# Performance work log

Hardware: AMD Instinct MI355X
Metric: run time of the kernel (lower is better)

Reference implementation:

```python
import jax, jax.numpy as jnp
import numpy as np

B, H, T1, T2, DK, DV = 4, 16, 1024, 1024, 64, 64


def setup_inputs() -> dict:
    key = jax.random.key(0)
    k1, k2, k3 = jax.random.split(key, 3)
    return {
        "query": jax.random.normal(k1, (B, H, T1, DK), dtype=jnp.float32),
        "key": jax.random.normal(k2, (B, T2, DK), dtype=jnp.float32),
        "value": jax.random.normal(k3, (B, T2, DV), dtype=jnp.float32),
        "mask": jnp.zeros((T1, T2), dtype=jnp.float32),
    }


def reference(query, key, value, mask):
    # logits = tanh(Q K^T): [B,H,T1,T2]; key broadcast over heads
    logits = jnp.tanh(jnp.einsum("bhqd,bkd->bhqk", query, key))
    logits = logits + mask  # additive positional mask [T1,T2]
    weights = jax.nn.softmax(logits, axis=-1)
    out = jnp.einsum("bhqk,bkv->bhqv", weights, value)
    return out, weights
```

## Files before the change

kernel.cpp:

```cpp
#include <hip/hip_runtime.h>


typedef _Float16 f16;
typedef __attribute__((ext_vector_type(2))) _Float16 f16x2;
typedef __attribute__((ext_vector_type(4))) _Float16 f16x4;
typedef __attribute__((ext_vector_type(8))) _Float16 f16x8;
typedef __attribute__((ext_vector_type(2))) __fp16  fp16x2;
typedef __attribute__((ext_vector_type(4))) float f32x4;

#define LOG2E 1.44269504088896340736f

union U8 { f16x8 v; f16x2 h[4]; };
union U4 { f16x4 v; f16x2 h[2]; };

static __device__ __forceinline__ f16x2 pk(float a, float b) {
  union { fp16x2 src; f16x2 dst; } u;
  u.src = __builtin_amdgcn_cvt_pkrtz(a, b);
  return u.dst;
}

static __device__ __forceinline__ void tanh_exp4(const f32x4& acc, const f32x4& m4,
                                                 float p[4]) {
  #pragma unroll
  for (int i = 0; i < 4; ++i) {
    float x = acc[i];
    float t = __builtin_amdgcn_exp2f(x * (2.0f * LOG2E));
    float r = __builtin_amdgcn_rcpf(t + 1.0f);
    p[i] = __builtin_amdgcn_exp2f(
               fmaf(m4[i], LOG2E, fmaf(r, -2.0f * LOG2E, LOG2E)));
  }
}

__global__ __launch_bounds__(256) void prep(
    const float* __restrict__ K, const float* __restrict__ V,
    const float* __restrict__ M,
    f16* __restrict__ Kp, f16* __restrict__ Vp, float* __restrict__ Mp)
{
  int idx = blockIdx.x * 256 + threadIdx.x;
  if (idx < 32768) {
    int l = idx & 63, ks = (idx >> 6) & 1, fc = (idx >> 7) & 63, b = idx >> 13;
    const float* s = K + ((size_t)b * 1024 + fc * 16 + (l & 15)) * 64
                       + (l >> 4) * 8 + ks * 32;
    f32x4 x = *(const f32x4*)s;
    f32x4 y = *(const f32x4*)(s + 4);
    U8 u;
    u.h[0] = pk(x[0], x[1]); u.h[1] = pk(x[2], x[3]);
    u.h[2] = pk(y[0], y[1]); u.h[3] = pk(y[2], y[3]);
    *(f16x8*)(Kp + (size_t)idx * 8) = u.v;
  } else if (idx < 98304) {
    int t = idx - 32768;
    int l = t & 63, nb = (t >> 6) & 3, fc = (t >> 8) & 63, b = t >> 14;
    const float* s = V + ((size_t)b * 1024 + fc * 16 + (l >> 4) * 4) * 64
                       + nb * 16 + (l & 15);
    U4 u;
    u.h[0] = pk(s[0],   s[64]);
    u.h[1] = pk(s[128], s[192]);
    *(f16x4*)(Vp + (size_t)t * 4) = u.v;
  } else if (idx < 360448) {
    int t = idx - 98304;
    int l = t & 63, fc = (t >> 6) & 63, q16 = t >> 12;
    const float* s = M + ((size_t)q16 * 16 + (l & 15)) * 1024
                       + fc * 16 + (l >> 4) * 4;
    *(f32x4*)(Mp + (size_t)t * 4) = *(const f32x4*)s;
  }
}

__global__ __launch_bounds__(256, 4) void attn_main(
    const float* __restrict__ Q, const f16* __restrict__ Kp,
    const f16* __restrict__ Vp, const float* __restrict__ Mp,
    float* __restrict__ Out, float* __restrict__ W)
{
  const int bh   = blockIdx.x >> 4;
  const int qt   = blockIdx.x & 15;
  const int b    = bh >> 4;
  const int lane = threadIdx.x & 63;
  const int wv   = threadIdx.x >> 6;
  const int qv   = lane & 15;
  const int g    = lane >> 4;
  const int qbase = qt * 64 + wv * 16;

  const float* qp = Q + ((size_t)(bh * 1024 + qbase + qv)) * 64 + g * 8;
  f16x8 bq[2];
  #pragma unroll
  for (int ks = 0; ks < 2; ++ks) {
    f32x4 a = *(const f32x4*)(qp + ks * 32);
    f32x4 c = *(const f32x4*)(qp + ks * 32 + 4);
    U8 u;
    u.h[0] = pk(a[0], a[1]); u.h[1] = pk(a[2], a[3]);
    u.h[2] = pk(c[0], c[1]); u.h[3] = pk(c[2], c[3]);
    bq[ks] = u.v;
  }

  const f16*   kpB = Kp + (size_t)b * 65536 + lane * 8;
  const f16*   vpB = Vp + (size_t)b * 65536 + lane * 4;
  const float* mpB = Mp + (size_t)(qt * 4 + wv) * 16384 + lane * 4;

  float rsum = 0.0f;
  f32x4 oacc[4];
  #pragma unroll
  for (int nb = 0; nb < 4; ++nb) oacc[nb] = f32x4{0.f, 0.f, 0.f, 0.f};

  #pragma unroll 2
  for (int fc = 0; fc < 64; ++fc) {
    f16x8 a0 = *(const f16x8*)(kpB + fc * 1024);
    f16x8 a1 = *(const f16x8*)(kpB + fc * 1024 + 512);
    f32x4 acc = {0.f, 0.f, 0.f, 0.f};
    acc = __builtin_amdgcn_mfma_f32_16x16x32_f16(a0, bq[0], acc, 0, 0, 0);
    acc = __builtin_amdgcn_mfma_f32_16x16x32_f16(a1, bq[1], acc, 0, 0, 0);

    f32x4 m4 = *(const f32x4*)(mpB + fc * 256);
    float p[4];
    tanh_exp4(acc, m4, p);
    rsum += (p[0] + p[1]) + (p[2] + p[3]);

    U4 pu;
    pu.h[0] = pk(p[0], p[1]);
    pu.h[1] = pk(p[2], p[3]);

    #pragma unroll
    for (int nb = 0; nb < 4; ++nb) {
      f16x4 bv = *(const f16x4*)(vpB + fc * 1024 + nb * 256);
      oacc[nb] = __builtin_amdgcn_mfma_f32_16x16x16f16(pu.v, bv, oacc[nb], 0, 0, 0);
    }
  }

  rsum += __shfl_xor(rsum, 16);
  rsum += __shfl_xor(rsum, 32);
  const float rz = 1.0f / rsum;
  float rzq[4];
  #pragma unroll
  for (int i = 0; i < 4; ++i) rzq[i] = __shfl(rz, g * 4 + i);

  float* ol = Out + ((size_t)(bh * 1024 + qbase)) * 64 + qv;
  #pragma unroll
  for (int nb = 0; nb < 4; ++nb) {
    #pragma unroll
    for (int i = 0; i < 4; ++i) {
      ol[(size_t)(g * 4 + i) * 64 + nb * 16] = oacc[nb][i] * rzq[i];
    }
  }

  float* wl = W + ((size_t)(bh * 1024 + qbase + qv)) * 1024 + g * 4;
  #pragma unroll 4
  for (int fc = 0; fc < 64; ++fc) {
    f16x8 a0 = *(const f16x8*)(kpB + fc * 1024);
    f16x8 a1 = *(const f16x8*)(kpB + fc * 1024 + 512);
    f32x4 acc = {0.f, 0.f, 0.f, 0.f};
    acc = __builtin_amdgcn_mfma_f32_16x16x32_f16(a0, bq[0], acc, 0, 0, 0);
    acc = __builtin_amdgcn_mfma_f32_16x16x32_f16(a1, bq[1], acc, 0, 0, 0);

    f32x4 m4 = *(const f32x4*)(mpB + fc * 256);
    float p[4];
    tanh_exp4(acc, m4, p);

    f32x4 w4;
    w4[0] = p[0] * rz; w4[1] = p[1] * rz;
    w4[2] = p[2] * rz; w4[3] = p[3] * rz;
    *(f32x4*)(wl + fc * 16) = w4;
  }
}

__global__ __launch_bounds__(256, 4) void attn_fused(
    const float* __restrict__ Q, const float* __restrict__ K,
    const float* __restrict__ V, const float* __restrict__ M,
    float* __restrict__ Out, float* __restrict__ W)
{
  const int bh   = blockIdx.x >> 4;
  const int qt   = blockIdx.x & 15;
  const int b    = bh >> 4;
  const int lane = threadIdx.x & 63;
  const int wv   = threadIdx.x >> 6;
  const int qv   = lane & 15;
  const int g    = lane >> 4;
  const int qbase = qt * 64 + wv * 16;

  const float* qp = Q + ((size_t)(bh * 1024 + qbase + qv)) * 64 + g * 8;
  f16x8 bq[2];
  #pragma unroll
  for (int ks = 0; ks < 2; ++ks) {
    f32x4 a = *(const f32x4*)(qp + ks * 32);
    f32x4 c = *(const f32x4*)(qp + ks * 32 + 4);
    U8 u;
    u.h[0] = pk(a[0], a[1]); u.h[1] = pk(a[2], a[3]);
    u.h[2] = pk(c[0], c[1]); u.h[3] = pk(c[2], c[3]);
    bq[ks] = u.v;
  }
  const float* kp = K + ((size_t)(b * 1024 + qv)) * 64 + g * 8;
  const float* mp = M + (size_t)(qbase + qv) * 1024 + g * 4;
  const float* vp = V + (size_t)b * 65536 + g * 256 + qv;

  float rsum = 0.0f;
  f32x4 oacc[4];
  #pragma unroll
  for (int nb = 0; nb < 4; ++nb) oacc[nb] = f32x4{0.f, 0.f, 0.f, 0.f};

  #pragma unroll 2
  for (int fc = 0; fc < 64; ++fc) {
    const float* kf = kp + fc * 1024;
    f16x8 ak[2];
    #pragma unroll
    for (int ks = 0; ks < 2; ++ks) {
      f32x4 a = *(const f32x4*)(kf + ks * 32);
      f32x4 c = *(const f32x4*)(kf + ks * 32 + 4);
      U8 u;
      u.h[0] = pk(a[0], a[1]); u.h[1] = pk(a[2], a[3]);
      u.h[2] = pk(c[0], c[1]); u.h[3] = pk(c[2], c[3]);
      ak[ks] = u.v;
    }
    f32x4 acc = {0.f, 0.f, 0.f, 0.f};
    acc = __builtin_amdgcn_mfma_f32_16x16x32_f16(ak[0], bq[0], acc, 0, 0, 0);
    acc = __builtin_amdgcn_mfma_f32_16x16x32_f16(ak[1], bq[1], acc, 0, 0, 0);
    f32x4 m4 = *(const f32x4*)(mp + fc * 16);
    float p[4];
    tanh_exp4(acc, m4, p);
    rsum += (p[0] + p[1]) + (p[2] + p[3]);
    U4 pu;
    pu.h[0] = pk(p[0], p[1]);
    pu.h[1] = pk(p[2], p[3]);
    const float* vf = vp + fc * 1024;
    #pragma unroll
    for (int nb = 0; nb < 4; ++nb) {
      U4 bu;
      bu.h[0] = pk(vf[nb * 16],       vf[nb * 16 + 64]);
      bu.h[1] = pk(vf[nb * 16 + 128], vf[nb * 16 + 192]);
      oacc[nb] = __builtin_amdgcn_mfma_f32_16x16x16f16(pu.v, bu.v, oacc[nb], 0, 0, 0);
    }
  }
  rsum += __shfl_xor(rsum, 16);
  rsum += __shfl_xor(rsum, 32);
  const float rz = 1.0f / rsum;
  float rzq[4];
  #pragma unroll
  for (int i = 0; i < 4; ++i) rzq[i] = __shfl(rz, g * 4 + i);
  float* ol = Out + ((size_t)(bh * 1024 + qbase)) * 64 + qv;
  #pragma unroll
  for (int nb = 0; nb < 4; ++nb)
    #pragma unroll
    for (int i = 0; i < 4; ++i)
      ol[(size_t)(g * 4 + i) * 64 + nb * 16] = oacc[nb][i] * rzq[i];

  float* wl = W + ((size_t)(bh * 1024 + qbase + qv)) * 1024 + g * 4;
  #pragma unroll 2
  for (int fc = 0; fc < 64; ++fc) {
    const float* kf = kp + fc * 1024;
    f16x8 ak[2];
    #pragma unroll
    for (int ks = 0; ks < 2; ++ks) {
      f32x4 a = *(const f32x4*)(kf + ks * 32);
      f32x4 c = *(const f32x4*)(kf + ks * 32 + 4);
      U8 u;
      u.h[0] = pk(a[0], a[1]); u.h[1] = pk(a[2], a[3]);
      u.h[2] = pk(c[0], c[1]); u.h[3] = pk(c[2], c[3]);
      ak[ks] = u.v;
    }
    f32x4 acc = {0.f, 0.f, 0.f, 0.f};
    acc = __builtin_amdgcn_mfma_f32_16x16x32_f16(ak[0], bq[0], acc, 0, 0, 0);
    acc = __builtin_amdgcn_mfma_f32_16x16x32_f16(ak[1], bq[1], acc, 0, 0, 0);
    f32x4 m4 = *(const f32x4*)(mp + fc * 16);
    float p[4];
    tanh_exp4(acc, m4, p);
    f32x4 w4;
    w4[0] = p[0] * rz; w4[1] = p[1] * rz;
    w4[2] = p[2] * rz; w4[3] = p[3] * rz;
    *(f32x4*)(wl + fc * 16) = w4;
  }
}

extern "C" void kernel_launch(void* const* d_in, const int* in_sizes, int n_in,
                              void* d_out, int out_size, void* d_ws, size_t ws_size,
                              hipStream_t stream) {
  const float* Q = (const float*)d_in[0];
  const float* K = (const float*)d_in[1];
  const float* V = (const float*)d_in[2];
  const float* M = (const float*)d_in[3];
  float* Out = (float*)d_out;
  float* W   = Out + (size_t)4 * 16 * 1024 * 64;

  const size_t KP_BYTES = 524288, VP_BYTES = 524288, MP_BYTES = 4194304;
  if (ws_size >= KP_BYTES + VP_BYTES + MP_BYTES) {
    f16*   Kp = (f16*)d_ws;
    f16*   Vp = (f16*)((char*)d_ws + KP_BYTES);
    float* Mp = (float*)((char*)d_ws + KP_BYTES + VP_BYTES);
    hipLaunchKernelGGL(prep, dim3(1408), dim3(256), 0, stream, K, V, M, Kp, Vp, Mp);
    hipLaunchKernelGGL(attn_main, dim3(1024), dim3(256), 0, stream,
                       Q, Kp, Vp, Mp, Out, W);
  } else {
    hipLaunchKernelGGL(attn_fused, dim3(1024), dim3(256), 0, stream,
                       Q, K, V, M, Out, W);
  }
}
```

Before: 374.7 us.

## Split attention into row-sum kernel and fused weights-plus-PV pass

Moves the softmax denominator computation into its own kernel that writes per-row reciprocal sums to workspace. The second kernel then computes logits once, writing normalized weights and accumulating the PV product in the same loop, instead of accumulating PV in one loop and recomputing logits for the weights in another. The QK/tanh/exp work per element is unchanged (still done twice overall), but the weight stores now interleave with the MFMA PV work, and the cost is an extra kernel launch plus a small workspace buffer and an extra Q load. The fast path now needs slightly more workspace, so the fallback may trigger if the workspace is too small.

```diff
diff --git a/kernel.cpp b/kernel.cpp
--- a/kernel.cpp
+++ b/kernel.cpp
@@ -28,6 +28,18 @@
     float r = __builtin_amdgcn_rcpf(t + 1.0f);
     p[i] = __builtin_amdgcn_exp2f(
                fmaf(m4[i], LOG2E, fmaf(r, -2.0f * LOG2E, LOG2E)));
+  }
+}
+
+static __device__ __forceinline__ void load_bq(const float* qp, f16x8 bq[2]) {
+  #pragma unroll
+  for (int ks = 0; ks < 2; ++ks) {
+    f32x4 a = *(const f32x4*)(qp + ks * 32);
+    f32x4 c = *(const f32x4*)(qp + ks * 32 + 4);
+    U8 u;
+    u.h[0] = pk(a[0], a[1]); u.h[1] = pk(a[2], a[3]);
+    u.h[2] = pk(c[0], c[1]); u.h[3] = pk(c[2], c[3]);
+    bq[ks] = u.v;
   }
 }
 
@@ -65,9 +77,47 @@
   }
 }
 
-__global__ __launch_bounds__(256, 4) void attn_main(
+__global__ __launch_bounds__(256, 4) void attn_rsum(
+    const float* __restrict__ Q, const f16* __restrict__ Kp,
+    const float* __restrict__ Mp, float* __restrict__ Rz)
+{
+  const int bh   = blockIdx.x >> 4;
+  const int qt   = blockIdx.x & 15;
+  const int b    = bh >> 4;
+  const int lane = threadIdx.x & 63;
+  const int wv   = threadIdx.x >> 6;
+  const int qv   = lane & 15;
+  const int qbase = qt * 64 + wv * 16;
+
+  const float* qp = Q + ((size_t)(bh * 1024 + qbase + qv)) * 64 + (lane >> 4) * 8;
+  f16x8 bq[2];
+  load_bq(qp, bq);
+
+  const f16*   kpB = Kp + (size_t)b * 65536 + lane * 8;
+  const float* mpB = Mp + (size_t)(qt * 4 + wv) * 16384 + lane * 4;
+
+  float rsum = 0.0f;
+  #pragma unroll 4
+  for (int fc = 0; fc < 64; ++fc) {
+    f16x8 a0 = *(const f16x8*)(kpB + fc * 1024);
+    f16x8 a1 = *(const f16x8*)(kpB + fc * 1024 + 512);
+    f32x4 acc = {0.f, 0.f, 0.f, 0.f};
+    acc = __builtin_amdgcn_mfma_f32_16x16x32_f16(a0, bq[0], acc, 0, 0, 0);
+    acc = __builtin_amdgcn_mfma_f32_16x16x32_f16(a1, bq[1], acc, 0, 0, 0);
+    f32x4 m4 = *(const f32x4*)(mpB + fc * 256);
+    float p[4];
+    tanh_exp4(acc, m4, p);
+    rsum += (p[0] + p[1]) + (p[2] + p[3]);
+  }
+  rsum += __shfl_xor(rsum, 16);
+  rsum += __shfl_xor(rsum, 32);
+  if (lane < 16) Rz[bh * 1024 + qbase + lane] = 1.0f / rsum;
+}
+
+__global__ __launch_bounds__(256, 4) void attn_pass2(
     const float* __restrict__ Q, const f16* __restrict__ Kp,
     const f16* __restrict__ Vp, const float* __restrict__ Mp,
+    const float* __restrict__ Rz,
     float* __restrict__ Out, float* __restrict__ W)
 {
   const int bh   = blockIdx.x >> 4;
@@ -81,21 +131,18 @@
 
   const float* qp = Q + ((size_t)(bh * 1024 + qbase + qv)) * 64 + g * 8;
   f16x8 bq[2];
-  #pragma unroll
-  for (int ks = 0; ks < 2; ++ks) {
-    f32x4 a = *(const f32x4*)(qp + ks * 32);
-    f32x4 c = *(const f32x4*)(qp + ks * 32 + 4);
-    U8 u;
-    u.h[0] = pk(a[0], a[1]); u.h[1] = pk(a[2], a[3]);
-    u.h[2] = pk(c[0], c[1]); u.h[3] = pk(c[2], c[3]);
-    bq[ks] = u.v;
-  }
+  load_bq(qp, bq);
 
   const f16*   kpB = Kp + (size_t)b * 65536 + lane * 8;
   const f16*   vpB = Vp + (size_t)b * 65536 + lane * 4;
   const float* mpB = Mp + (size_t)(qt * 4 + wv) * 16384 + lane * 4;
 
-  float rsum = 0.0f;
+  const float rz = Rz[bh * 1024 + qbase + qv];
+  float rzq[4];
+  #pragma unroll
+  for (int i = 0; i < 4; ++i) rzq[i] = __shfl(rz, g * 4 + i);
+
+  float* wl = W + ((size_t)(bh * 1024 + qbase + qv)) * 1024 + g * 4;
   f32x4 oacc[4];
   #pragma unroll
   for (int nb = 0; nb < 4; ++nb) oacc[nb] = f32x4{0.f, 0.f, 0.f, 0.f};
@@ -111,52 +158,29 @@
     f32x4 m4 = *(const f32x4*)(mpB + fc * 256);
     float p[4];
     tanh_exp4(acc, m4, p);
-    rsum += (p[0] + p[1]) + (p[2] + p[3]);
-
-    U4 pu;
-    pu.h[0] = pk(p[0], p[1]);
-    pu.h[1] = pk(p[2], p[3]);
-
-    #pragma unroll
-    for (int nb = 0; nb < 4; ++nb) {
-      f16x4 bv = *(const f16x4*)(vpB + fc * 1024 + nb * 256);
-      oacc[nb] = __builtin_amdgcn_mfma_f32_16x16x16f16(pu.v, bv, oacc[nb], 0, 0, 0);
-    }
-  }
-
-  rsum += __shfl_xor(rsum, 16);
-  rsum += __shfl_xor(rsum, 32);
-  const float rz = 1.0f / rsum;
-  float rzq[4];
-  #pragma unroll
-  for (int i = 0; i < 4; ++i) rzq[i] = __shfl(rz, g * 4 + i);
-
-  float* ol = Out + ((size_t)(bh * 1024 + qbase)) * 64 + qv;
-  #pragma unroll
-  for (int nb = 0; nb < 4; ++nb) {
-    #pragma unroll
-    for (int i = 0; i < 4; ++i) {
-      ol[(size_t)(g * 4 + i) * 64 + nb * 16] = oacc[nb][i] * rzq[i];
-    }
-  }
-
-  float* wl = W + ((size_t)(bh * 1024 + qbase + qv)) * 1024 + g * 4;
-  #pragma unroll 4
-  for (int fc = 0; fc < 64; ++fc) {
-    f16x8 a0 = *(const f16x8*)(kpB + fc * 1024);
-    f16x8 a1 = *(const f16x8*)(kpB + fc * 1024 + 512);
-    f32x4 acc = {0.f, 0.f, 0.f, 0.f};
-    acc = __builtin_amdgcn_mfma_f32_16x16x32_f16(a0, bq[0], acc, 0, 0, 0);
-    acc = __builtin_amdgcn_mfma_f32_16x16x32_f16(a1, bq[1], acc, 0, 0, 0);
-
-    f32x4 m4 = *(const f32x4*)(mpB + fc * 256);
-    float p[4];
-    tanh_exp4(acc, m4, p);
 
     f32x4 w4;
     w4[0] = p[0] * rz; w4[1] = p[1] * rz;
     w4[2] = p[2] * rz; w4[3] = p[3] * rz;
     *(f32x4*)(wl + fc * 16) = w4;
+
+    U4 pu;
+    pu.h[0] = pk(p[0], p[1]);
+    pu.h[1] = pk(p[2], p[3]);
+    #pragma unroll
+    for (int nb = 0; nb < 4; ++nb) {
+      f16x4 bv = *(const f16x4*)(vpB + fc * 1024 + nb * 256);
+      oacc[nb] = __builtin_amdgcn_mfma_f32_16x16x16f16(pu.v, bv, oacc[nb], 0, 0, 0);
+    }
+  }
+
+  float* ol = Out + ((size_t)(bh * 1024 + qbase)) * 64 + qv;
+  #pragma unroll
+  for (int nb = 0; nb < 4; ++nb) {
+    #pragma unroll
+    for (int i = 0; i < 4; ++i) {
+      ol[(size_t)(g * 4 + i) * 64 + nb * 16] = oacc[nb][i] * rzq[i];
+    }
   }
 }
 
@@ -176,15 +200,7 @@
 
   const float* qp = Q + ((size_t)(bh * 1024 + qbase + qv)) * 64 + g * 8;
   f16x8 bq[2];
-  #pragma unroll
-  for (int ks = 0; ks < 2; ++ks) {
-    f32x4 a = *(const f32x4*)(qp + ks * 32);
-    f32x4 c = *(const f32x4*)(qp + ks * 32 + 4);
-    U8 u;
-    u.h[0] = pk(a[0], a[1]); u.h[1] = pk(a[2], a[3]);
-    u.h[2] = pk(c[0], c[1]); u.h[3] = pk(c[2], c[3]);
-    bq[ks] = u.v;
-  }
+  load_bq(qp, bq);
   const float* kp = K + ((size_t)(b * 1024 + qv)) * 64 + g * 8;
   const float* mp = M + (size_t)(qbase + qv) * 1024 + g * 4;
   const float* vp = V + (size_t)b * 65536 + g * 256 + qv;
@@ -276,14 +292,17 @@
   float* Out = (float*)d_out;
   float* W   = Out + (size_t)4 * 16 * 1024 * 64;
 
-  const size_t KP_BYTES = 524288, VP_BYTES = 524288, MP_BYTES = 4194304;
-  if (ws_size >= KP_BYTES + VP_BYTES + MP_BYTES) {
+  const size_t KP_BYTES = 524288, VP_BYTES = 524288, MP_BYTES = 4194304,
+               RZ_BYTES = 262144;
+  if (ws_size >= KP_BYTES + VP_BYTES + MP_BYTES + RZ_BYTES) {
     f16*   Kp = (f16*)d_ws;
     f16*   Vp = (f16*)((char*)d_ws + KP_BYTES);
     float* Mp = (float*)((char*)d_ws + KP_BYTES + VP_BYTES);
+    float* Rz = (float*)((char*)d_ws + KP_BYTES + VP_BYTES + MP_BYTES);
     hipLaunchKernelGGL(prep, dim3(1408), dim3(256), 0, stream, K, V, M, Kp, Vp, Mp);
-    hipLaunchKernelGGL(attn_main, dim3(1024), dim3(256), 0, stream,
-                       Q, Kp, Vp, Mp, Out, W);
+    hipLaunchKernelGGL(attn_rsum, dim3(1024), dim3(256), 0, stream, Q, Kp, Mp, Rz);
+    hipLaunchKernelGGL(attn_pass2, dim3(1024), dim3(256), 0, stream,
+                       Q, Kp, Vp, Mp, Rz, Out, W);
   } else {
     hipLaunchKernelGGL(attn_fused, dim3(1024), dim3(256), 0, stream,
                        Q, K, V, M, Out, W);
```

New measurement: 384.2 us. +2.5%, slower.

## Split key range across two wave groups per block with LDS reduction

Applied to the files above, without the earlier changes.

Doubles the block to 512 threads so each 16-query subtile is handled by two waves, each covering half of the key chunks. Partial row sums and output accumulators are combined through shared memory after a barrier, and each half then writes its own part of the weights. The goal is more waves in flight and a shorter serial loop per wave. The cost is extra LDS traffic, a block-wide synchronization, and K/V fragments being loaded by more waves.

```diff
diff --git a/kernel.cpp b/kernel.cpp
--- a/kernel.cpp
+++ b/kernel.cpp
@@ -28,6 +28,18 @@
     float r = __builtin_amdgcn_rcpf(t + 1.0f);
     p[i] = __builtin_amdgcn_exp2f(
                fmaf(m4[i], LOG2E, fmaf(r, -2.0f * LOG2E, LOG2E)));
+  }
+}
+
+static __device__ __forceinline__ void load_bq(const float* qp, f16x8 bq[2]) {
+  #pragma unroll
+  for (int ks = 0; ks < 2; ++ks) {
+    f32x4 a = *(const f32x4*)(qp + ks * 32);
+    f32x4 c = *(const f32x4*)(qp + ks * 32 + 4);
+    U8 u;
+    u.h[0] = pk(a[0], a[1]); u.h[1] = pk(a[2], a[3]);
+    u.h[2] = pk(c[0], c[1]); u.h[3] = pk(c[2], c[3]);
+    bq[ks] = u.v;
   }
 }
 
@@ -65,35 +77,33 @@
   }
 }
 
-__global__ __launch_bounds__(256, 4) void attn_main(
+__global__ __launch_bounds__(512, 6) void attn_main2(
     const float* __restrict__ Q, const f16* __restrict__ Kp,
     const f16* __restrict__ Vp, const float* __restrict__ Mp,
     float* __restrict__ Out, float* __restrict__ W)
 {
+  __shared__ float redO[8][16][64];
+  __shared__ float redS[8][16];
+
   const int bh   = blockIdx.x >> 4;
   const int qt   = blockIdx.x & 15;
   const int b    = bh >> 4;
   const int lane = threadIdx.x & 63;
-  const int wv   = threadIdx.x >> 6;
+  const int ww   = threadIdx.x >> 6;
+  const int sub  = ww & 3;
+  const int kh   = ww >> 2;
   const int qv   = lane & 15;
   const int g    = lane >> 4;
-  const int qbase = qt * 64 + wv * 16;
+  const int qbase = qt * 64 + sub * 16;
+  const int fc0 = kh * 32, fc1 = fc0 + 32;
 
   const float* qp = Q + ((size_t)(bh * 1024 + qbase + qv)) * 64 + g * 8;
   f16x8 bq[2];
-  #pragma unroll
-  for (int ks = 0; ks < 2; ++ks) {
-    f32x4 a = *(const f32x4*)(qp + ks * 32);
-    f32x4 c = *(const f32x4*)(qp + ks * 32 + 4);
-    U8 u;
-    u.h[0] = pk(a[0], a[1]); u.h[1] = pk(a[2], a[3]);
-    u.h[2] = pk(c[0], c[1]); u.h[3] = pk(c[2], c[3]);
-    bq[ks] = u.v;
-  }
+  load_bq(qp, bq);
 
   const f16*   kpB = Kp + (size_t)b * 65536 + lane * 8;
   const f16*   vpB = Vp + (size_t)b * 65536 + lane * 4;
-  const float* mpB = Mp + (size_t)(qt * 4 + wv) * 16384 + lane * 4;
+  const float* mpB = Mp + (size_t)(qt * 4 + sub) * 16384 + lane * 4;
 
   float rsum = 0.0f;
   f32x4 oacc[4];
@@ -101,7 +111,7 @@
   for (int nb = 0; nb < 4; ++nb) oacc[nb] = f32x4{0.f, 0.f, 0.f, 0.f};
 
   #pragma unroll 2
-  for (int fc = 0; fc < 64; ++fc) {
+  for (int fc = fc0; fc < fc1; ++fc) {
     f16x8 a0 = *(const f16x8*)(kpB + fc * 1024);
     f16x8 a1 = *(const f16x8*)(kpB + fc * 1024 + 512);
     f32x4 acc = {0.f, 0.f, 0.f, 0.f};
@@ -116,7 +126,6 @@
     U4 pu;
     pu.h[0] = pk(p[0], p[1]);
     pu.h[1] = pk(p[2], p[3]);
-
     #pragma unroll
     for (int nb = 0; nb < 4; ++nb) {
       f16x4 bv = *(const f16x4*)(vpB + fc * 1024 + nb * 256);
@@ -126,23 +135,35 @@
 
   rsum += __shfl_xor(rsum, 16);
   rsum += __shfl_xor(rsum, 32);
-  const float rz = 1.0f / rsum;
-  float rzq[4];
-  #pragma unroll
-  for (int i = 0; i < 4; ++i) rzq[i] = __shfl(rz, g * 4 + i);
-
-  float* ol = Out + ((size_t)(bh * 1024 + qbase)) * 64 + qv;
-  #pragma unroll
-  for (int nb = 0; nb < 4; ++nb) {
-    #pragma unroll
-    for (int i = 0; i < 4; ++i) {
-      ol[(size_t)(g * 4 + i) * 64 + nb * 16] = oacc[nb][i] * rzq[i];
+
+  if (lane < 16) redS[ww][lane] = rsum;
+  #pragma unroll
+  for (int nb = 0; nb < 4; ++nb)
+    #pragma unroll
+    for (int i = 0; i < 4; ++i)
+      redO[ww][nb * 4 + i][lane] = oacc[nb][i];
+  __syncthreads();
+
+  const float rz = 1.0f / (redS[sub][qv] + redS[sub + 4][qv]);
+
+  if (kh == 0) {
+    float rzq[4];
+    #pragma unroll
+    for (int i = 0; i < 4; ++i) rzq[i] = __shfl(rz, g * 4 + i);
+    float* ol = Out + ((size_t)(bh * 1024 + qbase)) * 64 + qv;
+    #pragma unroll
+    for (int nb = 0; nb < 4; ++nb) {
+      #pragma unroll
+      for (int i = 0; i < 4; ++i) {
+        float o = oacc[nb][i] + redO[ww + 4][nb * 4 + i][lane];
+        ol[(size_t)(g * 4 + i) * 64 + nb * 16] = o * rzq[i];
+      }
     }
   }
 
   float* wl = W + ((size_t)(bh * 1024 + qbase + qv)) * 1024 + g * 4;
   #pragma unroll 4
-  for (int fc = 0; fc < 64; ++fc) {
+  for (int fc = fc0; fc < fc1; ++fc) {
     f16x8 a0 = *(const f16x8*)(kpB + fc * 1024);
     f16x8 a1 = *(const f16x8*)(kpB + fc * 1024 + 512);
     f32x4 acc = {0.f, 0.f, 0.f, 0.f};
@@ -176,15 +197,7 @@
 
   const float* qp = Q + ((size_t)(bh * 1024 + qbase + qv)) * 64 + g * 8;
   f16x8 bq[2];
-  #pragma unroll
-  for (int ks = 0; ks < 2; ++ks) {
-    f32x4 a = *(const f32x4*)(qp + ks * 32);
-    f32x4 c = *(const f32x4*)(qp + ks * 32 + 4);
-    U8 u;
-    u.h[0] = pk(a[0], a[1]); u.h[1] = pk(a[2], a[3]);
-    u.h[2] = pk(c[0], c[1]); u.h[3] = pk(c[2], c[3]);
-    bq[ks] = u.v;
-  }
+  load_bq(qp, bq);
   const float* kp = K + ((size_t)(b * 1024 + qv)) * 64 + g * 8;
   const float* mp = M + (size_t)(qbase + qv) * 1024 + g * 4;
   const float* vp = V + (size_t)b * 65536 + g * 256 + qv;
@@ -282,7 +295,7 @@
     f16*   Vp = (f16*)((char*)d_ws + KP_BYTES);
     float* Mp = (float*)((char*)d_ws + KP_BYTES + VP_BYTES);
     hipLaunchKernelGGL(prep, dim3(1408), dim3(256), 0, stream, K, V, M, Kp, Vp, Mp);
-    hipLaunchKernelGGL(attn_main, dim3(1024), dim3(256), 0, stream,
+    hipLaunchKernelGGL(attn_main2, dim3(1024), dim3(512), 0, stream,
                        Q, Kp, Vp, Mp, Out, W);
   } else {
     hipLaunchKernelGGL(attn_fused, dim3(1024), dim3(256), 0, stream,
```

Result: slower. 405.5 us (+8.2%).
